# Optimization experiments

Measured on AMD Instinct MI355X. Metric: run time of the kernel, lower is better.

## Reference

```python
import jax, jax.numpy as jnp
import numpy as np

VOCAB = 50257
H = 512  # output_size == embed dim == lstm hidden
N = 65536  # number of tokens


def setup_inputs() -> dict:
    key = jax.random.key(0)
    ks = jax.random.split(key, 12)
    s = 1.0 / np.sqrt(H)  # torch LSTM/Linear init scale
    inp = {
        "ids": jax.random.randint(ks[0], (N,), 0, VOCAB, dtype=jnp.int64)
        if jax.config.jax_enable_x64 else jax.random.randint(ks[0], (N,), 0, VOCAB, dtype=jnp.int32),
        "emb": jax.random.normal(ks[1], (VOCAB, H), dtype=jnp.float32),
        # LSTM layer 0 (gate order: i, f, g, o)
        "W_ih0": jax.random.uniform(ks[2], (4 * H, H), jnp.float32, -s, s),
        "W_hh0": jax.random.uniform(ks[3], (4 * H, H), jnp.float32, -s, s),
        "b_ih0": jax.random.uniform(ks[4], (4 * H,), jnp.float32, -s, s),
        "b_hh0": jax.random.uniform(ks[5], (4 * H,), jnp.float32, -s, s),
        # LSTM layer 1
        "W_ih1": jax.random.uniform(ks[6], (4 * H, H), jnp.float32, -s, s),
        "W_hh1": jax.random.uniform(ks[7], (4 * H, H), jnp.float32, -s, s),
        "b_ih1": jax.random.uniform(ks[8], (4 * H,), jnp.float32, -s, s),
        "b_hh1": jax.random.uniform(ks[9], (4 * H,), jnp.float32, -s, s),
        # final Linear
        "W_lin": jax.random.uniform(ks[10], (H, H), jnp.float32, -s, s),
        "b_lin": jax.random.uniform(ks[11], (H,), jnp.float32, -s, s),
    }
    return inp


def _lstm_cell_zero_state(x, W_ih, b_ih, b_hh):
    # Single LSTM step with h_prev = c_prev = 0, so W_hh @ h_prev == 0.
    # gates: [N, 4H] in torch order i, f, g, o
    gates = x @ W_ih.T + (b_ih + b_hh)
    i, f, g, o = jnp.split(gates, 4, axis=-1)
    c = jax.nn.sigmoid(i) * jnp.tanh(g)  # f * c_prev == 0
    h = jax.nn.sigmoid(o) * jnp.tanh(c)
    return h


def reference(ids, emb, W_ih0, W_hh0, b_ih0, b_hh0, W_ih1, W_hh1, b_ih1, b_hh1, W_lin, b_lin):
    # Each token is processed with a fresh zero LSTM state, so the python
    # loop in the original vectorizes exactly over the token dim.
    x = emb[ids]                                   # [N, H]
    h0 = _lstm_cell_zero_state(x, W_ih0, b_ih0, b_hh0)   # layer 1 hidden
    h1 = _lstm_cell_zero_state(h0, W_ih1, b_ih1, b_hh1)  # layer 2 hidden (hidden[-1])
    out = jax.nn.relu(h1 @ W_lin.T + b_lin)        # [N, H]
    return out[:, None, :]                         # stacked [N, 1, H] like torch.stack of [1,H]
```

## Files before the change

kernel.cpp:

```cpp
#include <hip/hip_runtime.h>
#include <stdint.h>


typedef _Float16 half8 __attribute__((ext_vector_type(8)));
typedef __attribute__((ext_vector_type(4))) float float4v;
typedef __attribute__((ext_vector_type(4))) unsigned int uint4v;

__device__ __forceinline__ float sigmoidf_(float x) { return 1.0f / (1.0f + __expf(-x)); }
__device__ __forceinline__ float tanhf_(float x) { return 1.0f - 2.0f / (__expf(2.0f * x) + 1.0f); }

__device__ __forceinline__ void gl2lds16(const void* g, void* l) {
  __builtin_amdgcn_global_load_lds(
      (const __attribute__((address_space(1))) void*)g,
      (__attribute__((address_space(3))) void*)l, 16, 0, 0);
}

__global__ __launch_bounds__(256) void prep_kernel(
    const float* __restrict__ emb,
    const float* __restrict__ W0, const float* __restrict__ bi0, const float* __restrict__ bh0,
    const float* __restrict__ W1, const float* __restrict__ bi1, const float* __restrict__ bh1,
    const float* __restrict__ WL,
    _Float16* __restrict__ Ef,
    _Float16* __restrict__ W0f, _Float16* __restrict__ W1f, _Float16* __restrict__ WLf,
    float* __restrict__ b0p, float* __restrict__ b1p)
{
  int id = blockIdx.x * 256 + threadIdx.x;
  if (id < 3216448) {
    const float* s = emb + (size_t)id * 8;
    float4v v0 = *(const float4v*)s;
    float4v v1 = *(const float4v*)(s + 4);
    union { _Float16 h[8]; uint4v u; } P;
#pragma unroll
    for (int e = 0; e < 4; ++e) { P.h[e] = (_Float16)v0[e]; P.h[4 + e] = (_Float16)v1[e]; }
    *(uint4v*)(Ef + (size_t)id * 8) = P.u;
  } else if (id < 3347520) {
    int u = id - 3216448;
    int np = u >> 6, k0 = (u & 63) << 3;
    int n = ((np & 3) << 9) | (np >> 2);
    const float* s = W0 + n * 512 + k0;
    float4v v0 = *(const float4v*)s;
    float4v v1 = *(const float4v*)(s + 4);
    union { _Float16 h[8]; uint4v u; } P;
#pragma unroll
    for (int e = 0; e < 4; ++e) { P.h[e] = (_Float16)v0[e]; P.h[4 + e] = (_Float16)v1[e]; }
    *(uint4v*)(W0f + np * 512 + k0) = P.u;
  } else if (id < 3478592) {
    int u = id - 3347520;
    int np = u >> 6, k0 = (u & 63) << 3;
    int n = ((np & 3) << 9) | (np >> 2);
    const float* s = W1 + n * 512 + k0;
    float4v v0 = *(const float4v*)s;
    float4v v1 = *(const float4v*)(s + 4);
    union { _Float16 h[8]; uint4v u; } P;
#pragma unroll
    for (int e = 0; e < 4; ++e) { P.h[e] = (_Float16)v0[e]; P.h[4 + e] = (_Float16)v1[e]; }
    *(uint4v*)(W1f + np * 512 + k0) = P.u;
  } else if (id < 3511360) {
    int u = id - 3478592;
    const float* s = WL + (size_t)u * 8;
    float4v v0 = *(const float4v*)s;
    float4v v1 = *(const float4v*)(s + 4);
    union { _Float16 h[8]; uint4v u8; } P;
#pragma unroll
    for (int e = 0; e < 4; ++e) { P.h[e] = (_Float16)v0[e]; P.h[4 + e] = (_Float16)v1[e]; }
    *(uint4v*)(WLf + (size_t)u * 8) = P.u8;
  } else if (id < 3513408) {
    int np = id - 3511360;
    int n = ((np & 3) << 9) | (np >> 2);
    b0p[np] = bi0[n] + bh0[n];
  } else if (id < 3515456) {
    int np = id - 3513408;
    int n = ((np & 3) << 9) | (np >> 2);
    b1p[np] = bi1[n] + bh1[n];
  }
}

template <int MODE>
__global__ __launch_bounds__(256, 2) void gemm_kernel(
    const _Float16* __restrict__ A, const int* __restrict__ ids,
    const _Float16* __restrict__ B, const float* __restrict__ bias,
    _Float16* __restrict__ Of, float* __restrict__ Out,
    int nbShift, int nbMask)
{
  __shared__ __align__(16) char smem[49152];
  const int T = threadIdx.x;
  const int lane = T & 63;
  const int wv = T >> 6;
  const int wrow = wv >> 1, wcol = wv & 1;

  const int nwg = (int)gridDim.x;
  const int bid = (int)blockIdx.x;
  const int swz = (bid & 7) * (nwg >> 3) + (bid >> 3);
  const int mb = swz >> nbShift;
  const int nb = swz & nbMask;
  const size_t t0 = (size_t)mb * 256;
  const int n0 = nb * 128;

  const int r0 = T >> 2;
  const int qg = (T & 3) ^ ((r0 >> 1) & 3);
  size_t ra0 = t0 + r0, ra1 = t0 + 64 + r0, ra2 = t0 + 128 + r0, ra3 = t0 + 192 + r0;
  if (ids) {
    ra0 = (size_t)(unsigned)ids[ra0]; ra1 = (size_t)(unsigned)ids[ra1];
    ra2 = (size_t)(unsigned)ids[ra2]; ra3 = (size_t)(unsigned)ids[ra3];
  }
  const _Float16* gA0 = A + ra0 * 512 + qg * 8;
  const _Float16* gA1 = A + ra1 * 512 + qg * 8;
  const _Float16* gA2 = A + ra2 * 512 + qg * 8;
  const _Float16* gA3 = A + ra3 * 512 + qg * 8;
  const _Float16* gB0 = B + (size_t)(n0 + r0) * 512 + qg * 8;
  const _Float16* gB1 = B + (size_t)(n0 + 64 + r0) * 512 + qg * 8;

  const int m_ = lane & 15, qf = lane >> 4;
  const int qs = qf ^ ((m_ >> 1) & 3);
  const int offA = (wrow * 128 + m_) * 32 + qs * 8;
  const int offB = (wcol * 64 + m_) * 32 + qs * 8;

  float4v acc[8][4];
#pragma unroll
  for (int i = 0; i < 8; ++i)
#pragma unroll
    for (int j = 0; j < 4; ++j)
      acc[i][j] = (float4v){0.f, 0.f, 0.f, 0.f};

  _Float16* sA0 = (_Float16*)smem;
  _Float16* sB0 = (_Float16*)(smem + 16384);
  _Float16* sA1 = (_Float16*)(smem + 24576);
  _Float16* sB1 = (_Float16*)(smem + 40960);

  gl2lds16(gA0, sA0 + T * 8);
  gl2lds16(gA1, sA0 + 2048 + T * 8);
  gl2lds16(gA2, sA0 + 4096 + T * 8);
  gl2lds16(gA3, sA0 + 6144 + T * 8);
  gl2lds16(gB0, sB0 + T * 8);
  gl2lds16(gB1, sB0 + 2048 + T * 8);
  gA0 += 32; gA1 += 32; gA2 += 32; gA3 += 32; gB0 += 32; gB1 += 32;

  const _Float16* sAc = sA0;
  const _Float16* sBc = sB0;
  _Float16* sAn = sA1;
  _Float16* sBn = sB1;

#pragma unroll 2
  for (int it = 0; it < 16; ++it) {
    if (it < 15) {
      gl2lds16(gA0, sAn + T * 8);
      gl2lds16(gA1, sAn + 2048 + T * 8);
      gl2lds16(gA2, sAn + 4096 + T * 8);
      gl2lds16(gA3, sAn + 6144 + T * 8);
      gl2lds16(gB0, sBn + T * 8);
      gl2lds16(gB1, sBn + 2048 + T * 8);
      gA0 += 32; gA1 += 32; gA2 += 32; gA3 += 32; gB0 += 32; gB1 += 32;
      asm volatile("s_waitcnt vmcnt(6)" ::: "memory");
    } else {
      asm volatile("s_waitcnt vmcnt(0)" ::: "memory");
    }
    __builtin_amdgcn_sched_barrier(0);
    __builtin_amdgcn_s_barrier();

    half8 a[8], b[4];
#pragma unroll
    for (int i = 0; i < 8; ++i) a[i] = *(const half8*)(sAc + offA + i * 512);
#pragma unroll
    for (int j = 0; j < 4; ++j) b[j] = *(const half8*)(sBc + offB + j * 512);
#pragma unroll
    for (int i = 0; i < 8; ++i)
#pragma unroll
      for (int j = 0; j < 4; ++j)
        acc[i][j] = __builtin_amdgcn_mfma_f32_16x16x32_f16(b[j], a[i], acc[i][j], 0, 0, 0);

    asm volatile("s_waitcnt lgkmcnt(0)" ::: "memory");
    __builtin_amdgcn_sched_barrier(0);
    __builtin_amdgcn_s_barrier();
    const _Float16* tA = sAc; sAc = sAn; sAn = (_Float16*)tA;
    const _Float16* tB = sBc; sBc = sBn; sBn = (_Float16*)tB;
  }

  float4v bq[4];
#pragma unroll
  for (int j = 0; j < 4; ++j)
    bq[j] = *(const float4v*)(bias + n0 + wcol * 64 + j * 16 + qf * 4);

  if (MODE == 0) {
    _Float16* hT = (_Float16*)smem;
    const int u0 = wcol * 16 + qf;
#pragma unroll
    for (int i = 0; i < 8; ++i) {
      const int trow = wrow * 128 + i * 16 + m_;
#pragma unroll
      for (int j = 0; j < 4; ++j) {
        float yi = acc[i][j][0] + bq[j][0];
        float yg = acc[i][j][2] + bq[j][2];
        float yo = acc[i][j][3] + bq[j][3];
        float cc = sigmoidf_(yi) * tanhf_(yg);
        float hh = sigmoidf_(yo) * tanhf_(cc);
        hT[trow * 40 + u0 + j * 4] = (_Float16)hh;
      }
    }
    __syncthreads();
    const _Float16* src = hT + T * 40;
    uint4v v0 = *(const uint4v*)(src);
    uint4v v1 = *(const uint4v*)(src + 8);
    uint4v v2 = *(const uint4v*)(src + 16);
    uint4v v3 = *(const uint4v*)(src + 24);
    _Float16* dst = Of + (t0 + T) * 512 + (size_t)(nb * 32);
    *(uint4v*)(dst) = v0;
    *(uint4v*)(dst + 8) = v1;
    *(uint4v*)(dst + 16) = v2;
    *(uint4v*)(dst + 24) = v3;
  } else {
#pragma unroll
    for (int i = 0; i < 8; ++i) {
      const size_t row = t0 + wrow * 128 + i * 16 + m_;
#pragma unroll
      for (int j = 0; j < 4; ++j) {
        float4v v;
#pragma unroll
        for (int r = 0; r < 4; ++r)
          v[r] = fmaxf(acc[i][j][r] + bq[j][r], 0.0f);
        *(float4v*)(Out + row * 512 + (size_t)(n0 + wcol * 64 + j * 16 + qf * 4)) = v;
      }
    }
  }
}

extern "C" void kernel_launch(void* const* d_in, const int* in_sizes, int n_in,
                              void* d_out, int out_size, void* d_ws, size_t ws_size,
                              hipStream_t stream) {
  (void)in_sizes; (void)n_in; (void)out_size; (void)ws_size;
  const int*   ids   = (const int*)d_in[0];
  const float* emb   = (const float*)d_in[1];
  const float* W0    = (const float*)d_in[2];
  const float* bi0   = (const float*)d_in[4];
  const float* bh0   = (const float*)d_in[5];
  const float* W1    = (const float*)d_in[6];
  const float* bi1   = (const float*)d_in[8];
  const float* bh1   = (const float*)d_in[9];
  const float* WL    = (const float*)d_in[10];
  const float* blin  = (const float*)d_in[11];
  float* out = (float*)d_out;

  char* ws = (char*)d_ws;
  const size_t MB = 1024 * 1024;
  _Float16* W0f = (_Float16*)(ws);
  _Float16* W1f = (_Float16*)(ws + 2 * MB);
  _Float16* WLf = (_Float16*)(ws + 4 * MB);
  float*    b0p = (float*)(ws + 4 * MB + 512 * 1024);
  float*    b1p = (float*)(ws + 4 * MB + 512 * 1024 + 8192);
  _Float16* Ef  = (_Float16*)(ws + 8 * MB);
  _Float16* H1f = Ef;
  _Float16* H0f = (_Float16*)(ws + 72 * MB);

  prep_kernel<<<13733, 256, 0, stream>>>(emb, W0, bi0, bh0, W1, bi1, bh1, WL,
                                         Ef, W0f, W1f, WLf, b0p, b1p);
  gemm_kernel<0><<<4096, 256, 0, stream>>>(Ef, ids, W0f, b0p, H0f, nullptr, 4, 15);
  gemm_kernel<0><<<4096, 256, 0, stream>>>(H0f, nullptr, W1f, b1p, H1f, nullptr, 4, 15);
  gemm_kernel<1><<<1024, 256, 0, stream>>>(H1f, nullptr, WLf, blin, nullptr, out, 2, 3);
}
```

Measured before the change: 648.2 us.

## Enlarge GEMM tile to 256x256 with 8 waves and restructured LDS pipeline

The GEMM kernel moves from 256-thread blocks computing 256x128 tiles to 512-thread blocks computing 256x256 tiles. This halves how often the A operand is reloaded per output column block. The main loop now reads fragments from LDS first and then issues the next global-to-LDS stage. The MFMA work is split into two halves separated by barriers, each raised with s_setprio, so load issue and compute interleave across waves. In exchange, occupancy drops to one block per CU with 64KB of LDS, and the extra barriers plus full vmcnt(0) waits may expose load latency.

```diff
diff --git a/kernel.cpp b/kernel.cpp
--- a/kernel.cpp
+++ b/kernel.cpp
@@ -76,17 +76,17 @@
 }
 
 template <int MODE>
-__global__ __launch_bounds__(256, 2) void gemm_kernel(
+__global__ __launch_bounds__(512, 1) void gemm_kernel(
     const _Float16* __restrict__ A, const int* __restrict__ ids,
     const _Float16* __restrict__ B, const float* __restrict__ bias,
     _Float16* __restrict__ Of, float* __restrict__ Out,
     int nbShift, int nbMask)
 {
-  __shared__ __align__(16) char smem[49152];
+  __shared__ __align__(16) char smem[65536];
   const int T = threadIdx.x;
   const int lane = T & 63;
   const int wv = T >> 6;
-  const int wrow = wv >> 1, wcol = wv & 1;
+  const int wrow = wv >> 2, wcol = wv & 3;
 
   const int nwg = (int)gridDim.x;
   const int bid = (int)blockIdx.x;
@@ -94,26 +94,30 @@
   const int mb = swz >> nbShift;
   const int nb = swz & nbMask;
   const size_t t0 = (size_t)mb * 256;
-  const int n0 = nb * 128;
-
-  const int r0 = T >> 2;
-  const int qg = (T & 3) ^ ((r0 >> 1) & 3);
-  size_t ra0 = t0 + r0, ra1 = t0 + 64 + r0, ra2 = t0 + 128 + r0, ra3 = t0 + 192 + r0;
+  const int n0 = nb * 256;
+
+  const int r = T >> 2;
+  const int qg = (T & 3) ^ ((r >> 1) & 3);
+  size_t ar0 = t0 + r, ar1 = t0 + 128 + r;
   if (ids) {
-    ra0 = (size_t)(unsigned)ids[ra0]; ra1 = (size_t)(unsigned)ids[ra1];
-    ra2 = (size_t)(unsigned)ids[ra2]; ra3 = (size_t)(unsigned)ids[ra3];
-  }
-  const _Float16* gA0 = A + ra0 * 512 + qg * 8;
-  const _Float16* gA1 = A + ra1 * 512 + qg * 8;
-  const _Float16* gA2 = A + ra2 * 512 + qg * 8;
-  const _Float16* gA3 = A + ra3 * 512 + qg * 8;
-  const _Float16* gB0 = B + (size_t)(n0 + r0) * 512 + qg * 8;
-  const _Float16* gB1 = B + (size_t)(n0 + 64 + r0) * 512 + qg * 8;
+    ar0 = (size_t)(unsigned)ids[ar0]; ar1 = (size_t)(unsigned)ids[ar1];
+  }
+  const _Float16* pA0 = A + ar0 * 512 + qg * 8;
+  const _Float16* pA1 = A + ar1 * 512 + qg * 8;
+  const _Float16* pB0 = B + (size_t)(n0 + r) * 512 + qg * 8;
+  const _Float16* pB1 = B + (size_t)(n0 + 128 + r) * 512 + qg * 8;
+
+  const int d0 = T * 16;
+
+#define STAGE(dst) do { \
+    gl2lds16(pA0, (dst) + d0);         gl2lds16(pA1, (dst) + 8192 + d0); \
+    gl2lds16(pB0, (dst) + 16384 + d0); gl2lds16(pB1, (dst) + 24576 + d0); \
+    pA0 += 32; pA1 += 32; pB0 += 32; pB1 += 32; } while (0)
 
   const int m_ = lane & 15, qf = lane >> 4;
   const int qs = qf ^ ((m_ >> 1) & 3);
   const int offA = (wrow * 128 + m_) * 32 + qs * 8;
-  const int offB = (wcol * 64 + m_) * 32 + qs * 8;
+  const int offB = 8192 + (wcol * 64 + m_) * 32 + qs * 8;
 
   float4v acc[8][4];
 #pragma unroll
@@ -122,58 +126,50 @@
     for (int j = 0; j < 4; ++j)
       acc[i][j] = (float4v){0.f, 0.f, 0.f, 0.f};
 
-  _Float16* sA0 = (_Float16*)smem;
-  _Float16* sB0 = (_Float16*)(smem + 16384);
-  _Float16* sA1 = (_Float16*)(smem + 24576);
-  _Float16* sB1 = (_Float16*)(smem + 40960);
-
-  gl2lds16(gA0, sA0 + T * 8);
-  gl2lds16(gA1, sA0 + 2048 + T * 8);
-  gl2lds16(gA2, sA0 + 4096 + T * 8);
-  gl2lds16(gA3, sA0 + 6144 + T * 8);
-  gl2lds16(gB0, sB0 + T * 8);
-  gl2lds16(gB1, sB0 + 2048 + T * 8);
-  gA0 += 32; gA1 += 32; gA2 += 32; gA3 += 32; gB0 += 32; gB1 += 32;
-
-  const _Float16* sAc = sA0;
-  const _Float16* sBc = sB0;
-  _Float16* sAn = sA1;
-  _Float16* sBn = sB1;
+  char* b0c = smem;
+  char* b1c = smem + 32768;
+  STAGE(b0c);
+  asm volatile("s_waitcnt vmcnt(0)" ::: "memory");
+  __builtin_amdgcn_sched_barrier(0);
+  __builtin_amdgcn_s_barrier();
+
+  const _Float16* cur = (const _Float16*)b0c;
+  char* nxt = b1c;
 
 #pragma unroll 2
-  for (int it = 0; it < 16; ++it) {
-    if (it < 15) {
-      gl2lds16(gA0, sAn + T * 8);
-      gl2lds16(gA1, sAn + 2048 + T * 8);
-      gl2lds16(gA2, sAn + 4096 + T * 8);
-      gl2lds16(gA3, sAn + 6144 + T * 8);
-      gl2lds16(gB0, sBn + T * 8);
-      gl2lds16(gB1, sBn + 2048 + T * 8);
-      gA0 += 32; gA1 += 32; gA2 += 32; gA3 += 32; gB0 += 32; gB1 += 32;
-      asm volatile("s_waitcnt vmcnt(6)" ::: "memory");
-    } else {
-      asm volatile("s_waitcnt vmcnt(0)" ::: "memory");
-    }
-    __builtin_amdgcn_sched_barrier(0);
+  for (int t = 0; t < 16; ++t) {
+    half8 a[8], b[4];
+#pragma unroll
+    for (int i = 0; i < 8; ++i) a[i] = *(const half8*)(cur + offA + i * 512);
+#pragma unroll
+    for (int j = 0; j < 4; ++j) b[j] = *(const half8*)(cur + offB + j * 512);
+    if (t < 15) STAGE(nxt);
     __builtin_amdgcn_s_barrier();
-
-    half8 a[8], b[4];
-#pragma unroll
-    for (int i = 0; i < 8; ++i) a[i] = *(const half8*)(sAc + offA + i * 512);
-#pragma unroll
-    for (int j = 0; j < 4; ++j) b[j] = *(const half8*)(sBc + offB + j * 512);
-#pragma unroll
-    for (int i = 0; i < 8; ++i)
-#pragma unroll
-      for (int j = 0; j < 4; ++j)
-        acc[i][j] = __builtin_amdgcn_mfma_f32_16x16x32_f16(b[j], a[i], acc[i][j], 0, 0, 0);
-
     asm volatile("s_waitcnt lgkmcnt(0)" ::: "memory");
     __builtin_amdgcn_sched_barrier(0);
+    __builtin_amdgcn_s_setprio(1);
+#pragma unroll
+    for (int i = 0; i < 8; ++i) {
+      acc[i][0] = __builtin_amdgcn_mfma_f32_16x16x32_f16(b[0], a[i], acc[i][0], 0, 0, 0);
+      acc[i][1] = __builtin_amdgcn_mfma_f32_16x16x32_f16(b[1], a[i], acc[i][1], 0, 0, 0);
+    }
+    __builtin_amdgcn_s_setprio(0);
+    __builtin_amdgcn_sched_barrier(0);
     __builtin_amdgcn_s_barrier();
-    const _Float16* tA = sAc; sAc = sAn; sAn = (_Float16*)tA;
-    const _Float16* tB = sBc; sBc = sBn; sBn = (_Float16*)tB;
-  }
+    __builtin_amdgcn_s_setprio(1);
+#pragma unroll
+    for (int i = 0; i < 8; ++i) {
+      acc[i][2] = __builtin_amdgcn_mfma_f32_16x16x32_f16(b[2], a[i], acc[i][2], 0, 0, 0);
+      acc[i][3] = __builtin_amdgcn_mfma_f32_16x16x32_f16(b[3], a[i], acc[i][3], 0, 0, 0);
+    }
+    __builtin_amdgcn_s_setprio(0);
+    __builtin_amdgcn_sched_barrier(0);
+    if (t < 15) { asm volatile("s_waitcnt vmcnt(0)" ::: "memory"); }
+    __builtin_amdgcn_sched_barrier(0);
+    __builtin_amdgcn_s_barrier();
+    const _Float16* tc = cur; cur = (const _Float16*)nxt; nxt = (char*)tc;
+  }
+#undef STAGE
 
   float4v bq[4];
 #pragma unroll
@@ -182,7 +178,7 @@
 
   if (MODE == 0) {
     _Float16* hT = (_Float16*)smem;
-    const int u0 = wcol * 16 + qf;
+    const int ub = wcol * 16 + qf;
 #pragma unroll
     for (int i = 0; i < 8; ++i) {
       const int trow = wrow * 128 + i * 16 + m_;
@@ -193,17 +189,18 @@
         float yo = acc[i][j][3] + bq[j][3];
         float cc = sigmoidf_(yi) * tanhf_(yg);
         float hh = sigmoidf_(yo) * tanhf_(cc);
-        hT[trow * 40 + u0 + j * 4] = (_Float16)hh;
+        hT[trow * 72 + ub + j * 4] = (_Float16)hh;
       }
     }
     __syncthreads();
-    const _Float16* src = hT + T * 40;
+    const int tok = T >> 1, hf = T & 1;
+    const _Float16* src = hT + tok * 72 + hf * 32;
     uint4v v0 = *(const uint4v*)(src);
     uint4v v1 = *(const uint4v*)(src + 8);
     uint4v v2 = *(const uint4v*)(src + 16);
     uint4v v3 = *(const uint4v*)(src + 24);
-    _Float16* dst = Of + (t0 + T) * 512 + (size_t)(nb * 32);
-    *(uint4v*)(dst) = v0;
+    _Float16* dst = Of + (t0 + tok) * 512 + (size_t)nb * 64 + hf * 32;
+    *(uint4v*)dst = v0;
     *(uint4v*)(dst + 8) = v1;
     *(uint4v*)(dst + 16) = v2;
     *(uint4v*)(dst + 24) = v3;
@@ -215,8 +212,8 @@
       for (int j = 0; j < 4; ++j) {
         float4v v;
 #pragma unroll
-        for (int r = 0; r < 4; ++r)
-          v[r] = fmaxf(acc[i][j][r] + bq[j][r], 0.0f);
+        for (int r2 = 0; r2 < 4; ++r2)
+          v[r2] = fmaxf(acc[i][j][r2] + bq[j][r2], 0.0f);
         *(float4v*)(Out + row * 512 + (size_t)(n0 + wcol * 64 + j * 16 + qf * 4)) = v;
       }
     }
@@ -252,7 +249,7 @@
 
   prep_kernel<<<13733, 256, 0, stream>>>(emb, W0, bi0, bh0, W1, bi1, bh1, WL,
                                          Ef, W0f, W1f, WLf, b0p, b1p);
-  gemm_kernel<0><<<4096, 256, 0, stream>>>(Ef, ids, W0f, b0p, H0f, nullptr, 4, 15);
-  gemm_kernel<0><<<4096, 256, 0, stream>>>(H0f, nullptr, W1f, b1p, H1f, nullptr, 4, 15);
-  gemm_kernel<1><<<1024, 256, 0, stream>>>(H1f, nullptr, WLf, blin, nullptr, out, 2, 3);
-}
+  gemm_kernel<0><<<2048, 512, 0, stream>>>(Ef, ids, W0f, b0p, H0f, nullptr, 3, 7);
+  gemm_kernel<0><<<2048, 512, 0, stream>>>(H0f, nullptr, W1f, b1p, H1f, nullptr, 3, 7);
+  gemm_kernel<1><<<512, 512, 0, stream>>>(H1f, nullptr, WLf, blin, nullptr, out, 1, 1);
+}
```

After: 665.0 us. 1.03x slower.
